# Optimization experiments

Measured on AMD Instinct MI355X. Metric: run time of the kernel, lower is better.

## Reference

```python
import jax, jax.numpy as jnp
import numpy as np

TOP_K = 6  # num_experts_per_tok


def setup_inputs() -> dict:
    key = jax.random.key(0)
    k1, k2, k3, k4, k5 = jax.random.split(key, 5)
    B, S, H = 2, 2048, 2048
    E, M = 28, 1408
    scale = 0.02
    return {
        "hidden_states": jax.random.normal(k1, (B, S, H), jnp.float32),
        "gate_weight": jax.random.normal(k2, (E, H), jnp.float32) * scale,
        "w_gate": jax.random.normal(k3, (E, H, M), jnp.float32) * scale,
        "w_up": jax.random.normal(k4, (E, H, M), jnp.float32) * scale,
        "w_down": jax.random.normal(k5, (E, M, H), jnp.float32) * scale,
    }


def reference(hidden_states, gate_weight, w_gate, w_up, w_down):
    """DeepseekMoE forward (inference path): top-k softmax gating + expert
    dispatch/combine. gate_weight: [E, H]; w_gate/w_up: [E, H, M]; w_down: [E, M, H]."""
    B, S, H = hidden_states.shape
    x = hidden_states.reshape(-1, H)          # [T, H]
    T = x.shape[0]
    E = gate_weight.shape[0]

    # --- MoEGate: softmax scores, top-k, normalize top-k probs ---
    logits = x @ gate_weight.T                # [T, E]
    scores = jax.nn.softmax(logits, axis=-1)
    topk_w, topk_idx = jax.lax.top_k(scores, TOP_K)  # [T, K]
    topk_w = topk_w / (topk_w.sum(axis=-1, keepdims=True) + 1e-20)

    # Dense per-(token, expert) combine weights (0 for non-selected experts).
    cw = jnp.zeros((T, E), x.dtype).at[jnp.arange(T)[:, None], topk_idx].add(topk_w)

    # --- Expert compute + combine, scanning over experts to bound memory ---
    def step(y, inp):
        wg, wu, wd, w_tok = inp               # [H,M], [H,M], [M,H], [T]
        h = jax.nn.silu(x @ wg) * (x @ wu)    # [T, M]
        return y + w_tok[:, None] * (h @ wd), None

    y0 = jnp.zeros_like(x)
    y, _ = jax.lax.scan(step, y0, (w_gate, w_up, w_down, cw.T))
    return y.reshape(B, S, H)
```

## Files before the change

kernel.cpp:

```cpp
#include <hip/hip_runtime.h>
#include <stdint.h>

#define T_TOK 4096
#define HDIM 2048
#define MDIM 1408
#define NEXP 28
#define TOPK 6
#define NPAIR (T_TOK*TOPK)

typedef unsigned short u16;
typedef short short8 __attribute__((ext_vector_type(8)));
typedef float f32x4 __attribute__((ext_vector_type(4)));

__device__ __forceinline__ u16 f2bf(float x){
  unsigned int u = __float_as_uint(x);
  u += 0x7fffu + ((u >> 16) & 1u);
  return (u16)(u >> 16);
}

__device__ __forceinline__ void gload16(const u16* g, u16* l){
  __builtin_amdgcn_global_load_lds((const __attribute__((address_space(1))) unsigned int*)g,
                                   (__attribute__((address_space(3))) unsigned int*)l,
                                   16, 0, 0);
}

__global__ __launch_bounds__(256) void cvt_kernel(const float* __restrict__ x,
                                                  u16* __restrict__ xb, int n8){
  int i = blockIdx.x*256 + threadIdx.x;
  if (i >= n8) return;
  const float4* s = (const float4*)x + (size_t)i*2;
  float4 a = s[0], b = s[1];
  unsigned int w0 = (unsigned)f2bf(a.x) | ((unsigned)f2bf(a.y)<<16);
  unsigned int w1 = (unsigned)f2bf(a.z) | ((unsigned)f2bf(a.w)<<16);
  unsigned int w2 = (unsigned)f2bf(b.x) | ((unsigned)f2bf(b.y)<<16);
  unsigned int w3 = (unsigned)f2bf(b.z) | ((unsigned)f2bf(b.w)<<16);
  uint4 o = {w0,w1,w2,w3};
  ((uint4*)xb)[i] = o;
}

__global__ __launch_bounds__(256) void transpose_cvt(const float* __restrict__ in,
                                                     u16* __restrict__ out, int K, int N){
  const int e = blockIdx.z;
  const int n0 = blockIdx.x*64, k0 = blockIdx.y*64;
  const float* src = in + ((size_t)e*K + k0)*N + n0;
  u16* dst = out + ((size_t)e*N + n0)*K + k0;
  __shared__ u16 td[64][65];
  const int tid = threadIdx.x;
  const int rk = tid>>4, rn = (tid&15)*4;
  #pragma unroll
  for (int i=0;i<4;i++){
    int k = rk + 16*i;
    float4 v = *(const float4*)(src + (size_t)k*N + rn);
    td[k][rn+0]=f2bf(v.x); td[k][rn+1]=f2bf(v.y);
    td[k][rn+2]=f2bf(v.z); td[k][rn+3]=f2bf(v.w);
  }
  __syncthreads();
  const int wn = tid>>4, wk = (tid&15)*4;
  #pragma unroll
  for (int i=0;i<4;i++){
    int n = wn + 16*i;
    unsigned int lo = (unsigned)td[wk+0][n] | ((unsigned)td[wk+1][n]<<16);
    unsigned int hi = (unsigned)td[wk+2][n] | ((unsigned)td[wk+3][n]<<16);
    uint2 o = {lo, hi};
    *(uint2*)(dst + (size_t)n*K + wk) = o;
  }
}

__global__ __launch_bounds__(256) void gate_kernel(const float* __restrict__ x,
                                                   const float* __restrict__ gw,
                                                   int* __restrict__ topk_idx,
                                                   float* __restrict__ topk_w,
                                                   int* __restrict__ counts){
  const int wave = threadIdx.x >> 6, lane = threadIdx.x & 63;
  const int t = blockIdx.x*4 + wave;
  const float* xr = x + (size_t)t*HDIM;
  float xv[32];
  #pragma unroll
  for (int i=0;i<32;i++) xv[i] = xr[lane + 64*i];
  float sc[NEXP];
  #pragma unroll
  for (int e=0;e<NEXP;e++){
    const float* g = gw + (size_t)e*HDIM + lane;
    float a = 0.f;
    #pragma unroll
    for (int i=0;i<32;i++) a += xv[i]*g[64*i];
    #pragma unroll
    for (int d=32; d>0; d>>=1) a += __shfl_xor(a, d);
    sc[e] = a;
  }
  float mx = sc[0];
  #pragma unroll
  for (int e=1;e<NEXP;e++) mx = fmaxf(mx, sc[e]);
  unsigned int mask=0; int bi[TOPK]; float bs[TOPK]; float bsum=0.f;
  #pragma unroll
  for (int k=0;k<TOPK;k++){
    float bm=-3.4e38f; int bj=0;
    #pragma unroll
    for (int e=0;e<NEXP;e++){
      bool ok = (((mask>>e)&1u)==0u) && (sc[e]>bm);
      bm = ok ? sc[e] : bm; bj = ok ? e : bj;
    }
    mask |= (1u<<bj);
    float s = expf(bm - mx);
    bi[k]=bj; bs[k]=s; bsum+=s;
  }
  if (lane==0){
    float inv = 1.f/(bsum + 1e-20f);
    #pragma unroll
    for (int k=0;k<TOPK;k++){
      topk_idx[t*TOPK+k]=bi[k];
      topk_w[t*TOPK+k]=bs[k]*inv;
      atomicAdd(&counts[bi[k]],1);
    }
  }
}

__global__ void scan_kernel(const int* __restrict__ counts, int* __restrict__ offsets,
                            int* __restrict__ cursor){
  int t = threadIdx.x;
  if (t < NEXP) cursor[t] = 0;
  if (t == 0){
    int s = 0;
    for (int e=0;e<NEXP;e++){ offsets[e]=s; s+=counts[e]; }
    offsets[NEXP]=s;
  }
}

__global__ __launch_bounds__(256) void fill_kernel(const int* __restrict__ topk_idx,
                                                   const float* __restrict__ topk_w,
                                                   const int* __restrict__ offsets,
                                                   int* __restrict__ cursor,
                                                   int* __restrict__ pair_token,
                                                   float* __restrict__ pair_w){
  int t = blockIdx.x*256 + threadIdx.x;
  if (t >= T_TOK) return;
  #pragma unroll
  for (int k=0;k<TOPK;k++){
    int e = topk_idx[t*TOPK+k];
    int pos = atomicAdd(&cursor[e],1);
    int p = offsets[e]+pos;
    pair_token[p]=t;
    pair_w[p]=topk_w[t*TOPK+k];
  }
}

template<int NB, bool GATHER, int EPI>
__global__ __launch_bounds__(256,2) void gemm2(
    const u16* __restrict__ Ab, const u16* __restrict__ B0, const u16* __restrict__ B1,
    u16* __restrict__ Hout, float* __restrict__ Out,
    const int* __restrict__ counts, const int* __restrict__ offsets,
    const int* __restrict__ pair_token, const float* __restrict__ pair_w,
    int K, int N)
{
  const int e = blockIdx.z;
  const int cnt = counts[e];
  const int row0 = blockIdx.y*128;
  if (row0 >= cnt) return;
  const int off = offsets[e];
  const int n0 = blockIdx.x*128;

  __shared__ u16 smem[(1+NB)*8192];

  const int tid = threadIdx.x;
  const int lane = tid&63, wid = tid>>6;
  const int wm = wid>>1, wn = wid&1;
  const int lrow = lane&15, lgrp = lane>>4;

  const u16* ap[4]; const u16* bp0[4]; const u16* bp1[4];
  #pragma unroll
  for (int i=0;i<4;i++){
    int c = tid + 256*i;
    int r = c>>3;
    int sc = (c&7) ^ (r&7);
    int pr = off + min(row0 + r, cnt-1);
    const u16* arow = GATHER ? (Ab + (size_t)pair_token[pr]*K) : (Ab + (size_t)pr*K);
    ap[i] = arow + sc*8;
    size_t brow = (size_t)e*N + (size_t)(n0 + r);
    bp0[i] = B0 + brow*K + sc*8;
    if (NB==2) bp1[i] = B1 + brow*K + sc*8;
  }

  int aoffs[2][4], boffs[2][4];
  #pragma unroll
  for (int kh=0;kh<2;kh++){
    #pragma unroll
    for (int f=0; f<4; f++){
      int mr = wm*64 + f*16 + lrow;
      aoffs[kh][f] = mr*64 + (((kh*4+lgrp) ^ (mr&7))*8);
      int nr = wn*64 + f*16 + lrow;
      boffs[kh][f] = nr*64 + (((kh*4+lgrp) ^ (nr&7))*8);
    }
  }

  f32x4 acc0[4][4] = {};
  f32x4 acc1[4][4] = {};

  for (int kt=0; kt<K; kt+=64){
    __syncthreads();
    #pragma unroll
    for (int i=0;i<4;i++){
      int ldo = (tid + 256*i)*8;
      gload16(ap[i] + kt, &smem[ldo]);
      gload16(bp0[i] + kt, &smem[8192 + ldo]);
      if (NB==2) gload16(bp1[i] + kt, &smem[16384 + ldo]);
    }
    __syncthreads();
    #pragma unroll
    for (int kh=0; kh<2; kh++){
      short8 af[4], b0f[4], b1f[4];
      #pragma unroll
      for (int f=0;f<4;f++){
        af[f]  = *(const short8*)&smem[aoffs[kh][f]];
        b0f[f] = *(const short8*)&smem[8192 + boffs[kh][f]];
        if (NB==2) b1f[f] = *(const short8*)&smem[16384 + boffs[kh][f]];
      }
      #pragma unroll
      for (int fm=0;fm<4;fm++){
        #pragma unroll
        for (int fn=0;fn<4;fn++){
          acc0[fm][fn] = __builtin_amdgcn_mfma_f32_16x16x32_bf16(af[fm], b0f[fn], acc0[fm][fn],0,0,0);
          if (NB==2)
            acc1[fm][fn] = __builtin_amdgcn_mfma_f32_16x16x32_bf16(af[fm], b1f[fn], acc1[fm][fn],0,0,0);
        }
      }
    }
  }

  #pragma unroll
  for (int fm=0;fm<4;fm++){
    #pragma unroll
    for (int j=0;j<4;j++){
      int grow = wm*64 + fm*16 + lgrp*4 + j;
      if (row0+grow < cnt){
        int p = off + row0 + grow;
        if (EPI==0){
          u16* hrow = Hout + (size_t)p*N;
          #pragma unroll
          for (int fn=0;fn<4;fn++){
            int col = n0 + wn*64 + fn*16 + lrow;
            float g = acc0[fm][fn][j], u = acc1[fm][fn][j];
            hrow[col] = f2bf(g*u/(1.f+expf(-g)));
          }
        } else {
          int tok = pair_token[p];
          float wgt = pair_w[p];
          float* orow = Out + (size_t)tok*N;
          #pragma unroll
          for (int fn=0;fn<4;fn++){
            int col = n0 + wn*64 + fn*16 + lrow;
            atomicAdd(orow + col, wgt*acc0[fm][fn][j]);
          }
        }
      }
    }
  }
}

extern "C" void kernel_launch(void* const* d_in, const int* in_sizes, int n_in,
                              void* d_out, int out_size, void* d_ws, size_t ws_size,
                              hipStream_t stream) {
  const float* x  = (const float*)d_in[0];
  const float* gw = (const float*)d_in[1];
  const float* wg = (const float*)d_in[2];
  const float* wu = (const float*)d_in[3];
  const float* wd = (const float*)d_in[4];
  float* out = (float*)d_out;

  const size_t WT_BYTES = (size_t)NEXP*MDIM*HDIM*2;

  char* p = (char*)d_ws;
  u16* wg_t = (u16*)p;
  u16* wd_t = (u16*)p;
  p += WT_BYTES;
  u16* wu_t = (u16*)p; p += WT_BYTES;
  u16* xb   = (u16*)p; p += (size_t)T_TOK*HDIM*2;
  u16* hbuf = (u16*)p; p += (size_t)NPAIR*MDIM*2;
  int*   topk_idx   = (int*)p;   p += NPAIR*4;
  float* topk_w     = (float*)p; p += NPAIR*4;
  int*   pair_token = (int*)p;   p += NPAIR*4;
  float* pair_w     = (float*)p; p += NPAIR*4;
  int*   counts     = (int*)p;   p += 128;
  int*   offsets    = (int*)p;   p += 128;
  int*   cursor     = (int*)p;   p += 128;

  hipMemsetAsync(counts, 0, 128, stream);
  cvt_kernel<<<T_TOK*HDIM/8/256, 256, 0, stream>>>(x, xb, T_TOK*HDIM/8);
  gate_kernel<<<T_TOK/4, 256, 0, stream>>>(x, gw, topk_idx, topk_w, counts);
  scan_kernel<<<1, 64, 0, stream>>>(counts, offsets, cursor);
  fill_kernel<<<T_TOK/256, 256, 0, stream>>>(topk_idx, topk_w, offsets, cursor, pair_token, pair_w);
  hipMemsetAsync(out, 0, (size_t)out_size*4, stream);

  transpose_cvt<<<dim3(MDIM/64, HDIM/64, NEXP), 256, 0, stream>>>(wg, wg_t, HDIM, MDIM);
  transpose_cvt<<<dim3(MDIM/64, HDIM/64, NEXP), 256, 0, stream>>>(wu, wu_t, HDIM, MDIM);

  gemm2<2,true,0><<<dim3(MDIM/128, T_TOK/128, NEXP), 256, 0, stream>>>(
      xb, wg_t, wu_t, hbuf, nullptr, counts, offsets, pair_token, pair_w, HDIM, MDIM);

  transpose_cvt<<<dim3(HDIM/64, MDIM/64, NEXP), 256, 0, stream>>>(wd, wd_t, MDIM, HDIM);

  gemm2<1,false,1><<<dim3(HDIM/128, T_TOK/128, NEXP), 256, 0, stream>>>(
      hbuf, wd_t, nullptr, nullptr, out, counts, offsets, pair_token, pair_w, MDIM, HDIM);
}
```

Before: 1.212 ms.

## Replace atomic scatter-add with bf16 pair buffer and gather combine kernel

After: 1.043 ms. -13.9%, faster.

```diff
diff --git a/kernel.cpp b/kernel.cpp
--- a/kernel.cpp
+++ b/kernel.cpp
@@ -16,6 +16,9 @@
   unsigned int u = __float_as_uint(x);
   u += 0x7fffu + ((u >> 16) & 1u);
   return (u16)(u >> 16);
+}
+__device__ __forceinline__ float bf2f(unsigned int h){
+  return __uint_as_float(h << 16);
 }
 
 __device__ __forceinline__ void gload16(const u16* g, u16* l){
@@ -55,14 +58,16 @@
     td[k][rn+2]=f2bf(v.z); td[k][rn+3]=f2bf(v.w);
   }
   __syncthreads();
-  const int wn = tid>>4, wk = (tid&15)*4;
-  #pragma unroll
-  for (int i=0;i<4;i++){
-    int n = wn + 16*i;
-    unsigned int lo = (unsigned)td[wk+0][n] | ((unsigned)td[wk+1][n]<<16);
-    unsigned int hi = (unsigned)td[wk+2][n] | ((unsigned)td[wk+3][n]<<16);
-    uint2 o = {lo, hi};
-    *(uint2*)(dst + (size_t)n*K + wk) = o;
+  const int k8 = (tid&7)*8;
+  #pragma unroll
+  for (int i=0;i<2;i++){
+    int n = (tid>>3) + 32*i;
+    unsigned int w[4];
+    #pragma unroll
+    for (int j=0;j<4;j++)
+      w[j] = (unsigned)td[k8+2*j][n] | ((unsigned)td[k8+2*j+1][n]<<16);
+    uint4 o = {w[0],w[1],w[2],w[3]};
+    *(uint4*)(dst + (size_t)n*K + k8) = o;
   }
 }
 
@@ -131,33 +136,39 @@
                                                    const int* __restrict__ offsets,
                                                    int* __restrict__ cursor,
                                                    int* __restrict__ pair_token,
-                                                   float* __restrict__ pair_w){
+                                                   int* __restrict__ pos){
   int t = blockIdx.x*256 + threadIdx.x;
   if (t >= T_TOK) return;
   #pragma unroll
   for (int k=0;k<TOPK;k++){
     int e = topk_idx[t*TOPK+k];
-    int pos = atomicAdd(&cursor[e],1);
-    int p = offsets[e]+pos;
+    int c = atomicAdd(&cursor[e],1);
+    int p = offsets[e]+c;
     pair_token[p]=t;
-    pair_w[p]=topk_w[t*TOPK+k];
-  }
-}
-
-template<int NB, bool GATHER, int EPI>
+    pos[t*TOPK+k]=p;
+  }
+}
+
+template<int NB, bool GATHER, int EPI, int NBN>
 __global__ __launch_bounds__(256,2) void gemm2(
     const u16* __restrict__ Ab, const u16* __restrict__ B0, const u16* __restrict__ B1,
-    u16* __restrict__ Hout, float* __restrict__ Out,
+    u16* __restrict__ Hout,
     const int* __restrict__ counts, const int* __restrict__ offsets,
-    const int* __restrict__ pair_token, const float* __restrict__ pair_w,
-    int K, int N)
+    const int* __restrict__ pair_token,
+    int K, int N, int cpx)
 {
-  const int e = blockIdx.z;
+  const int bid = blockIdx.x;
+  const int swz = (bid & 7)*cpx + (bid >> 3);
+  const int rb  = swz & 31;
+  const int rest = swz >> 5;
+  const int n0b = rest % NBN;
+  const int e   = rest / NBN;
+
   const int cnt = counts[e];
-  const int row0 = blockIdx.y*128;
+  const int row0 = rb*128;
   if (row0 >= cnt) return;
   const int off = offsets[e];
-  const int n0 = blockIdx.x*128;
+  const int n0 = n0b*128;
 
   __shared__ u16 smem[(1+NB)*8192];
 
@@ -233,27 +244,46 @@
       int grow = wm*64 + fm*16 + lgrp*4 + j;
       if (row0+grow < cnt){
         int p = off + row0 + grow;
-        if (EPI==0){
-          u16* hrow = Hout + (size_t)p*N;
-          #pragma unroll
-          for (int fn=0;fn<4;fn++){
-            int col = n0 + wn*64 + fn*16 + lrow;
+        u16* hrow = Hout + (size_t)p*N;
+        #pragma unroll
+        for (int fn=0;fn<4;fn++){
+          int col = n0 + wn*64 + fn*16 + lrow;
+          if (EPI==0){
             float g = acc0[fm][fn][j], u = acc1[fm][fn][j];
             hrow[col] = f2bf(g*u/(1.f+expf(-g)));
-          }
-        } else {
-          int tok = pair_token[p];
-          float wgt = pair_w[p];
-          float* orow = Out + (size_t)tok*N;
-          #pragma unroll
-          for (int fn=0;fn<4;fn++){
-            int col = n0 + wn*64 + fn*16 + lrow;
-            atomicAdd(orow + col, wgt*acc0[fm][fn][j]);
+          } else {
+            hrow[col] = f2bf(acc0[fm][fn][j]);
           }
         }
       }
     }
   }
+}
+
+__global__ __launch_bounds__(256) void combine_kernel(const u16* __restrict__ pairbuf,
+                                                      const int* __restrict__ pos,
+                                                      const float* __restrict__ topk_w,
+                                                      float* __restrict__ out){
+  const int t = blockIdx.x;
+  const int c = threadIdx.x*8;
+  float acc[8] = {};
+  #pragma unroll
+  for (int k=0;k<TOPK;k++){
+    int p = pos[t*TOPK+k];
+    float w = topk_w[t*TOPK+k];
+    uint4 v = *(const uint4*)&pairbuf[(size_t)p*HDIM + c];
+    unsigned int ws_[4] = {v.x,v.y,v.z,v.w};
+    #pragma unroll
+    for (int j=0;j<4;j++){
+      acc[2*j]   += w*bf2f(ws_[j]&0xffffu);
+      acc[2*j+1] += w*bf2f(ws_[j]>>16);
+    }
+  }
+  float4 o0 = {acc[0],acc[1],acc[2],acc[3]};
+  float4 o1 = {acc[4],acc[5],acc[6],acc[7]};
+  float* orow = out + (size_t)t*HDIM + c;
+  *(float4*)orow = o0;
+  *(float4*)(orow+4) = o1;
 }
 
 extern "C" void kernel_launch(void* const* d_in, const int* in_sizes, int n_in,
@@ -272,13 +302,15 @@
   u16* wg_t = (u16*)p;
   u16* wd_t = (u16*)p;
   p += WT_BYTES;
-  u16* wu_t = (u16*)p; p += WT_BYTES;
+  u16* wu_t    = (u16*)p;
+  u16* pairbuf = (u16*)p;
+  p += WT_BYTES;
   u16* xb   = (u16*)p; p += (size_t)T_TOK*HDIM*2;
   u16* hbuf = (u16*)p; p += (size_t)NPAIR*MDIM*2;
   int*   topk_idx   = (int*)p;   p += NPAIR*4;
   float* topk_w     = (float*)p; p += NPAIR*4;
   int*   pair_token = (int*)p;   p += NPAIR*4;
-  float* pair_w     = (float*)p; p += NPAIR*4;
+  int*   pos        = (int*)p;   p += NPAIR*4;
   int*   counts     = (int*)p;   p += 128;
   int*   offsets    = (int*)p;   p += 128;
   int*   cursor     = (int*)p;   p += 128;
@@ -287,17 +319,24 @@
   cvt_kernel<<<T_TOK*HDIM/8/256, 256, 0, stream>>>(x, xb, T_TOK*HDIM/8);
   gate_kernel<<<T_TOK/4, 256, 0, stream>>>(x, gw, topk_idx, topk_w, counts);
   scan_kernel<<<1, 64, 0, stream>>>(counts, offsets, cursor);
-  fill_kernel<<<T_TOK/256, 256, 0, stream>>>(topk_idx, topk_w, offsets, cursor, pair_token, pair_w);
-  hipMemsetAsync(out, 0, (size_t)out_size*4, stream);
+  fill_kernel<<<T_TOK/256, 256, 0, stream>>>(topk_idx, topk_w, offsets, cursor, pair_token, pos);
 
   transpose_cvt<<<dim3(MDIM/64, HDIM/64, NEXP), 256, 0, stream>>>(wg, wg_t, HDIM, MDIM);
   transpose_cvt<<<dim3(MDIM/64, HDIM/64, NEXP), 256, 0, stream>>>(wu, wu_t, HDIM, MDIM);
 
-  gemm2<2,true,0><<<dim3(MDIM/128, T_TOK/128, NEXP), 256, 0, stream>>>(
-      xb, wg_t, wu_t, hbuf, nullptr, counts, offsets, pair_token, pair_w, HDIM, MDIM);
+  {
+    int ntile = 32*(MDIM/128)*NEXP;
+    gemm2<2,true,0,(MDIM/128)><<<ntile, 256, 0, stream>>>(
+        xb, wg_t, wu_t, hbuf, counts, offsets, pair_token, HDIM, MDIM, ntile/8);
+  }
 
   transpose_cvt<<<dim3(HDIM/64, MDIM/64, NEXP), 256, 0, stream>>>(wd, wd_t, MDIM, HDIM);
 
-  gemm2<1,false,1><<<dim3(HDIM/128, T_TOK/128, NEXP), 256, 0, stream>>>(
-      hbuf, wd_t, nullptr, nullptr, out, counts, offsets, pair_token, pair_w, MDIM, HDIM);
-}
+  {
+    int ntile = 32*(HDIM/128)*NEXP;
+    gemm2<1,false,1,(HDIM/128)><<<ntile, 256, 0, stream>>>(
+        hbuf, wd_t, nullptr, pairbuf, counts, offsets, pair_token, MDIM, HDIM, ntile/8);
+  }
+
+  combine_kernel<<<T_TOK, 256, 0, stream>>>(pairbuf, pos, topk_w, out);
+}
```
